# Performance work log

Measured on AMD Instinct MI355X. Metric: run time of the kernel, lower is better.

The kernel has to match this reference:

```python
import jax, jax.numpy as jnp
import numpy as np
from jax import lax
from jax.scipy.linalg import solve_triangular

SR = 16000
FRAME_PERIOD = 80
FFT_LENGTH = 1024
WIN_MS = 30
EPS = 1e-05
DEFAULT_F0 = 150.0
B, T, N = 8, 320000, 4000

N_BAND = int(np.log2(SR / 600))  # 4
CUTOFF = [SR / 2 ** i for i in range(2, N_BAND + 1)]
CUTOFF.append(CUTOFF[-1])  # [4000, 2000, 1000, 1000]
SEG = [int(c * WIN_MS / 500 + 1.5) for c in CUTOFF]  # [241, 121, 61, 61]

_HHP_VALS = [0.00041447996898231424, 0.0007812505141729248, -0.0010917236836275842,
             -0.001986792567596759, 0.0020903896961562292, 0.004094057027284935,
             -0.0034025808529816698, -0.007496154127205602, 0.004972263339933064,
             0.012738791249119802, -0.006696032689574911, -0.020694051570247052,
             0.008432436565041345, 0.03307438375870053, -0.010018936738799522,
             -0.05423136140580825, 0.011293988915051487, 0.10020081367388213,
             -0.012120546202484579, -0.316300210390957, 0.5124068258062764]
_HLP_VALS = [-0.0006548817007748305, 7.561994958159384e-05, 0.0020408456937895227,
             -0.0007468053532203044, -0.004350223568826493, 0.0025966428382642732,
             0.007639602282756696, -0.006490411890149785, -0.011765804538954506,
             0.013649908479276255, 0.01636866479016021, -0.026075976030529347,
             -0.020910294856659444, 0.04826072503231665, 0.02476784661104811,
             -0.09617846758336064, -0.027359756709866623, 0.3148805216163004,
             0.5282734359405503]

def _qmf_high():
    h = np.zeros(41)
    h[:21] = _HHP_VALS
    h[21:] = h[19::-1]
    return h.astype(np.float32)

def _qmf_low():
    h = np.zeros(37)
    h[:19] = _HLP_VALS
    h[19:] = h[17::-1]
    return h.astype(np.float32)

def _make_window():
    w = np.zeros((N_BAND, SEG[0]), np.float32)
    for i, s in enumerate(SEG):
        w[i, :s] = np.hanning(s + 2)[1:-1]
    return w

def _interp_tables():
    coarse = np.concatenate([[0.0], [SR / 2 ** i for i in range(N_BAND, 0, -1)]])
    freq = np.arange(FFT_LENGTH // 2 + 1) * (SR / FFT_LENGTH)
    idx = np.clip(np.searchsorted(coarse, freq) - 1, 0, len(coarse) - 2)
    x0 = coarse[:-1]
    dx = coarse[1:] - x0
    wts = ((freq - x0[idx]) / dx[idx]).astype(np.float32)
    return idx.astype(np.int32), wts

_HHP = _qmf_high()
_HLP = _qmf_low()
_WIN = _make_window()
_IDX, _WTS = _interp_tables()


def _qmf_conv(x, h):
    # x: (B, T), h: (k,). Reflection pad k//2, cross-correlation, stride 2.
    p = h.shape[0] // 2
    xp = jnp.pad(x, ((0, 0), (p, p)), mode='reflect')
    out = lax.conv_general_dilated(xp[:, None, :], h[None, None, :], (2,), 'VALID',
                                   dimension_numbers=('NCH', 'OIH', 'NCH'))
    return out[:, 0, :]


def setup_inputs() -> dict:
    key = jax.random.key(0)
    k1, k2 = jax.random.split(key)
    x = jax.random.normal(k1, (B, T), jnp.float32)
    f0 = 100.0 + 200.0 * jax.random.uniform(k2, (B, N), jnp.float32)  # 100-300 Hz
    return {"x": x, "f0": f0}


def reference(x, f0):
    hHP = jnp.asarray(_HHP)
    hLP = jnp.asarray(_HLP)
    f0 = lax.stop_gradient(jnp.where(f0 <= 32, DEFAULT_F0, f0))
    Bn, Nf = f0.shape
    time_axis = jnp.arange(Nf, dtype=f0.dtype) * (FRAME_PERIOD / SR)
    bidx = jnp.arange(Bn)[:, None, None]
    eye6 = EPS * jnp.eye(6, dtype=x.dtype)
    lx = x
    bap = []
    for i in range(N_BAND):
        if i < N_BAND - 1:
            hx = _qmf_conv(lx, hHP)
            lx = _qmf_conv(lx, hLP)
            xb = hx
        else:
            xb = lx
        seg = SEG[i]
        tmp_fs = 2.0 * CUTOFF[i]
        pitch = tmp_fs / f0
        t0 = (pitch + 0.5).astype(jnp.int32)
        index_bias = (pitch * 0.5 + 0.5).astype(jnp.int32)
        curr_pos = (time_axis * tmp_fs + 1.5).astype(jnp.int32)[None, :]
        origin = curr_pos - index_bias  # (B, N)
        j = jnp.arange(-1, seg + 1)  # (seg+2,)
        T1 = xb.shape[-1] - 1
        ia = jnp.clip((origin - t0)[..., None] + j, 0, T1)
        ib = jnp.clip((origin + t0)[..., None] + j, 0, T1)
        Ha = xb[bidx, ia]  # (B, N, seg+2)
        Hb = xb[bidx, ib]

        def unfold3(a):  # size-3 sliding windows -> (B, N, seg, 3)
            return jnp.stack([a[..., 0:seg], a[..., 1:seg + 1], a[..., 2:seg + 2]], axis=-1)

        H = jnp.concatenate([unfold3(Ha), unfold3(Hb)], axis=-1)  # (B, N, seg, 6)
        w = jnp.asarray(_WIN[i, :seg])
        Hw = jnp.swapaxes(H, -2, -1) * w  # (B, N, 6, seg)
        R = Hw @ H  # (B, N, 6, 6)
        ig = jnp.clip(origin[..., None] + j[1:-1], 0, T1)
        X = xb[bidx, ig][..., None]  # (B, N, seg, 1)
        L = jnp.linalg.cholesky(R + eye6)
        b = Hw @ X  # (B, N, 6, 1)
        y1 = solve_triangular(L, b, lower=True)
        a = solve_triangular(jnp.swapaxes(L, -2, -1), y1, lower=False)
        HaX = H @ a  # (B, N, seg, 1)
        wsqrt = jnp.sqrt(w)
        wx = wsqrt * X[..., 0]
        wxHa = wsqrt * (X - HaX)[..., 0]
        A = jnp.std(wxHa, axis=-1, ddof=1) / (jnp.std(wx, axis=-1, ddof=1) + 1e-16)
        bap.append(A)
    bap.append(bap[-1])
    ap = jnp.stack(bap[::-1], axis=-1)  # (B, N, n_band+1), low->high freq
    # piecewise-linear interpolation in log domain onto fft bins
    y = jnp.log(ap)
    y0 = y[..., :-1]
    dy = y[..., 1:] - y0
    yi = jnp.take(dy, jnp.asarray(_IDX), axis=-1) * jnp.asarray(_WTS) \
         + jnp.take(y0, jnp.asarray(_IDX), axis=-1)
    return jnp.exp(yi)  # (B, N, fft//2+1)
```

## Files before the change

kernel.cpp:

```cpp
#include <hip/hip_runtime.h>
#include <math.h>

#define NB 8
#define NF 4000
#define NFRAMES (NB * NF)

__constant__ float c_hhp[21] = {
    0.00041447996898231424, 0.0007812505141729248, -0.0010917236836275842,
    -0.001986792567596759,  0.0020903896961562292, 0.004094057027284935,
    -0.0034025808529816698, -0.007496154127205602, 0.004972263339933064,
    0.012738791249119802,   -0.006696032689574911, -0.020694051570247052,
    0.008432436565041345,   0.03307438375870053,   -0.010018936738799522,
    -0.05423136140580825,   0.011293988915051487,  0.10020081367388213,
    -0.012120546202484579,  -0.316300210390957,    0.5124068258062764};
__constant__ float c_hlp[19] = {
    -0.0006548817007748305, 7.561994958159384e-05, 0.0020408456937895227,
    -0.0007468053532203044, -0.004350223568826493, 0.0025966428382642732,
    0.007639602282756696,   -0.006490411890149785, -0.011765804538954506,
    0.013649908479276255,   0.01636866479016021,   -0.026075976030529347,
    -0.020910294856659444,  0.04826072503231665,   0.02476784661104811,
    -0.09617846758336064,   -0.027359756709866623, 0.3148805216163004,
    0.5282734359405503};

__device__ __forceinline__ int reflidx(int i, int len) {
  if (i < 0) i = -i;
  if (i >= len) i = 2 * len - 2 - i;
  return i;
}
__device__ __forceinline__ int clampi(int i, int hi) {
  return min(max(i, 0), hi);
}

__global__ __launch_bounds__(256) void qmf_kernel(
    const float* __restrict__ in, int len, float* __restrict__ outH,
    float* __restrict__ outL, float2* __restrict__ wtab) {
  int half = len >> 1;
  int gid = blockIdx.x * 256 + threadIdx.x;
  if (gid >= NB * half) {
    if (wtab) {
      const int segs[4] = {241, 121, 61, 61};
      int k = threadIdx.x;
      for (int i = 0; i < 4; ++i) {
        float v = 0.f;
        if (k < segs[i]) {
          double ang = 2.0 * 3.14159265358979323846 * (double)(k + 1) /
                       (double)(segs[i] + 1);
          v = (float)(0.5 - 0.5 * cos(ang));
        }
        wtab[i * 256 + k] = make_float2(v, sqrtf(v));
      }
    }
    return;
  }
  int b = gid / half;
  int nn = gid - b * half;
  const float* row = in + (size_t)b * len;
  int c = 2 * nn;
  float sh = 0.f, sl = 0.f;
  if (c >= 20 && c <= len - 22) {
    const float2* p2 = reinterpret_cast<const float2*>(row + (c - 20));
    float v[42];
#pragma unroll
    for (int j = 0; j < 21; ++j) {
      float2 t = p2[j];
      v[2 * j] = t.x;
      v[2 * j + 1] = t.y;
    }
#pragma unroll
    for (int t = 0; t < 41; ++t) sh += v[t] * c_hhp[t <= 20 ? t : 40 - t];
#pragma unroll
    for (int t = 0; t < 37; ++t) sl += v[t + 2] * c_hlp[t <= 18 ? t : 36 - t];
  } else {
#pragma unroll
    for (int t = 0; t < 41; ++t)
      sh += row[reflidx(c + t - 20, len)] * c_hhp[t <= 20 ? t : 40 - t];
#pragma unroll
    for (int t = 0; t < 37; ++t)
      sl += row[reflidx(c + t - 18, len)] * c_hlp[t <= 18 ? t : 36 - t];
  }
  outH[(size_t)b * half + nn] = sh;
  outL[(size_t)b * half + nn] = sl;
}

#define ACCUM_SAMPLE()                         \
  do {                                         \
    sxx += wk * x * x;                         \
    s1x += wsk * x;                            \
    float wh0 = wk * h0, wh1 = wk * h1, wh2 = wk * h2, wh3 = wk * h3, \
          wh4 = wk * h4, wh5 = wk * h5;        \
    gv[0] += wsk * h0; gv[1] += wsk * h1; gv[2] += wsk * h2;          \
    gv[3] += wsk * h3; gv[4] += wsk * h4; gv[5] += wsk * h5;          \
    bv[0] += wh0 * x;  bv[1] += wh1 * x;  bv[2] += wh2 * x;           \
    bv[3] += wh3 * x;  bv[4] += wh4 * x;  bv[5] += wh5 * x;           \
    rr[0] += wh0 * h0;  rr[1] += wh0 * h1;  rr[2] += wh0 * h2;        \
    rr[3] += wh0 * h3;  rr[4] += wh0 * h4;  rr[5] += wh0 * h5;        \
    rr[6] += wh1 * h1;  rr[7] += wh1 * h2;  rr[8] += wh1 * h3;        \
    rr[9] += wh1 * h4;  rr[10] += wh1 * h5; rr[11] += wh2 * h2;       \
    rr[12] += wh2 * h3; rr[13] += wh2 * h4; rr[14] += wh2 * h5;       \
    rr[15] += wh3 * h3; rr[16] += wh3 * h4; rr[17] += wh3 * h5;       \
    rr[18] += wh4 * h4; rr[19] += wh4 * h5; rr[20] += wh5 * h5;       \
  } while (0)

template <int GS, int NITER, bool CLAMP>
__device__ __forceinline__ void acc_loop(
    const float* __restrict__ row, int T1, int base_a, int base_b, int origin,
    int sub, const float2* __restrict__ wtab, float rr[21], float bv[6],
    float gv[6], float& sxx, float& s1x) {
  if (!CLAMP) {
    const float* pa = row + base_a + sub;
    const float* pb = row + base_b + sub;
    const float* pg = row + origin + sub;
    const float2* pw = wtab + sub;
#pragma unroll 4
    for (int j = 0; j < NITER; ++j) {
      float2 wp = pw[j * GS];
      float wk = wp.x, wsk = wp.y;
      float h0 = pa[j * GS], h1 = pa[j * GS + 1], h2 = pa[j * GS + 2];
      float h3 = pb[j * GS], h4 = pb[j * GS + 1], h5 = pb[j * GS + 2];
      float x = pg[j * GS];
      ACCUM_SAMPLE();
    }
  } else {
#pragma unroll 4
    for (int j = 0; j < NITER; ++j) {
      int k = sub + j * GS;
      float2 wp = wtab[k];
      float wk = wp.x, wsk = wp.y;
      int ia = base_a + k, ib = base_b + k;
      float h0 = row[clampi(ia, T1)];
      float h1 = row[clampi(ia + 1, T1)];
      float h2 = row[clampi(ia + 2, T1)];
      float h3 = row[clampi(ib, T1)];
      float h4 = row[clampi(ib + 1, T1)];
      float h5 = row[clampi(ib + 2, T1)];
      float x = row[clampi(origin + k, T1)];
      ACCUM_SAMPLE();
    }
  }
}

template <int SEG, int LGS, int NITER>
__device__ __forceinline__ void band_body(
    const float* __restrict__ xb, int bandLen, const float* __restrict__ f0,
    float tmp_fs, const float2* __restrict__ wtab, float* __restrict__ Aout,
    int blk) {
  constexpr int GS = 1 << LGS;
  constexpr int FPB = 256 / GS;
  constexpr int KMAX = NITER * GS;
  const int sub = threadIdx.x & (GS - 1);
  const int frame = blk * FPB + (threadIdx.x >> LGS);
  const int b = frame / NF;
  const int n = frame - b * NF;

  float f0v = f0[frame];
  if (f0v <= 32.0f) f0v = 150.0f;
  float pitch = tmp_fs / f0v;
  int t0 = (int)(__fadd_rn(pitch, 0.5f));
  int ibias = (int)(__fadd_rn(__fmul_rn(pitch, 0.5f), 0.5f));
  float tt = __fmul_rn((float)n, 0.005f);
  int curr = (int)(__fadd_rn(__fmul_rn(tt, tmp_fs), 1.5f));
  int origin = curr - ibias;
  const int T1 = bandLen - 1;
  const float* row = xb + (size_t)b * bandLen;
  const int base_a = origin - t0 - 1;
  const int base_b = origin + t0 - 1;

  float rr[21], bv[6], gv[6], sxx = 0.f, s1x = 0.f;
#pragma unroll
  for (int i = 0; i < 21; ++i) rr[i] = 0.f;
#pragma unroll
  for (int i = 0; i < 6; ++i) bv[i] = 0.f;
#pragma unroll
  for (int i = 0; i < 6; ++i) gv[i] = 0.f;

  const bool fast = (base_a >= 0) && (base_b + KMAX + 1 <= T1);
  if (fast)
    acc_loop<GS, NITER, false>(row, T1, base_a, base_b, origin, sub, wtab, rr,
                               bv, gv, sxx, s1x);
  else
    acc_loop<GS, NITER, true>(row, T1, base_a, base_b, origin, sub, wtab, rr,
                              bv, gv, sxx, s1x);

#pragma unroll
  for (int off = GS / 2; off >= 1; off >>= 1) {
#pragma unroll
    for (int i = 0; i < 21; ++i) rr[i] += __shfl_xor(rr[i], off, 64);
#pragma unroll
    for (int i = 0; i < 6; ++i) bv[i] += __shfl_xor(bv[i], off, 64);
    sxx += __shfl_xor(sxx, off, 64);
    s1x += __shfl_xor(s1x, off, 64);
  }

  float M[6][6], invd[6];
  {
    int c = 0;
#pragma unroll
    for (int p = 0; p < 6; ++p)
#pragma unroll
      for (int q = p; q < 6; ++q) {
        M[p][q] = rr[c];
        M[q][p] = rr[c];
        ++c;
      }
#pragma unroll
    for (int p = 0; p < 6; ++p) M[p][p] += 1e-5f;
  }
#pragma unroll
  for (int p = 0; p < 6; ++p) {
    float d = M[p][p];
#pragma unroll
    for (int j = 0; j < 6; ++j)
      if (j < p) d -= M[p][j] * M[p][j];
    d = sqrtf(d);
    M[p][p] = d;
    float inv = 1.0f / d;
    invd[p] = inv;
#pragma unroll
    for (int q = 0; q < 6; ++q)
      if (q > p) {
        float s = M[q][p];
#pragma unroll
        for (int j = 0; j < 6; ++j)
          if (j < p) s -= M[q][j] * M[p][j];
        M[q][p] = s * inv;
      }
  }
  float yv[6], av[6];
#pragma unroll
  for (int p = 0; p < 6; ++p) {
    float s = bv[p];
#pragma unroll
    for (int j = 0; j < 6; ++j)
      if (j < p) s -= M[p][j] * yv[j];
    yv[p] = s * invd[p];
  }
#pragma unroll
  for (int p = 5; p >= 0; --p) {
    float s = yv[p];
#pragma unroll
    for (int j = 0; j < 6; ++j)
      if (j > p) s -= M[j][p] * av[j];
    av[p] = s * invd[p];
  }

  float adotg = av[0] * gv[0] + av[1] * gv[1] + av[2] * gv[2] +
                av[3] * gv[3] + av[4] * gv[4] + av[5] * gv[5];
#pragma unroll
  for (int off = GS / 2; off >= 1; off >>= 1)
    adotg += __shfl_xor(adotg, off, 64);

  float adotb = 0.f, quad = 0.f;
  {
    int c = 0;
#pragma unroll
    for (int p = 0; p < 6; ++p) {
      adotb += av[p] * bv[p];
#pragma unroll
      for (int q = p; q < 6; ++q) {
        float t = av[p] * av[q] * rr[c++];
        quad += (q == p) ? t : 2.f * t;
      }
    }
  }
  if (sub == 0) {
    float s2r = sxx - 2.f * adotb + quad;
    float s1r = s1x - adotg;
    const float nf = (float)SEG;
    float vx = (sxx - s1x * s1x / nf) / (nf - 1.0f);
    float vr = (s2r - s1r * s1r / nf) / (nf - 1.0f);
    float sx = sqrtf(fmaxf(vx, 0.f));
    float sr = sqrtf(fmaxf(vr, 0.f));
    Aout[frame] = sr / (sx + 1e-16f);
  }
}

__global__ __launch_bounds__(256) void bands_kernel(
    const float* __restrict__ hx0, const float* __restrict__ hx1,
    const float* __restrict__ hx2, const float* __restrict__ lx2,
    const float* __restrict__ f0, const float2* __restrict__ wtab,
    float* __restrict__ Aarr) {
  int blk = blockIdx.x;
  if (blk < 1000) {
    band_body<241, 3, 32>(hx0, 160000, f0, 8000.0f, wtab + 0 * 256,
                          Aarr + 0 * NFRAMES, blk);
  } else if (blk < 2000) {
    band_body<121, 3, 16>(hx1, 80000, f0, 4000.0f, wtab + 1 * 256,
                          Aarr + 1 * NFRAMES, blk - 1000);
  } else if (blk < 2500) {
    band_body<61, 2, 16>(hx2, 40000, f0, 2000.0f, wtab + 2 * 256,
                         Aarr + 2 * NFRAMES, blk - 2000);
  } else {
    band_body<61, 2, 16>(lx2, 40000, f0, 2000.0f, wtab + 3 * 256,
                         Aarr + 3 * NFRAMES, blk - 2500);
  }
}

__global__ __launch_bounds__(256) void interp_kernel(
    const float* __restrict__ A, float* __restrict__ out) {
  const int wave = threadIdx.x >> 6;
  const int lane = threadIdx.x & 63;
  const int f = blockIdx.x * 4 + wave;
  float l0 = __logf(A[0 * NFRAMES + f]);
  float l1 = __logf(A[1 * NFRAMES + f]);
  float l2 = __logf(A[2 * NFRAMES + f]);
  float l3 = __logf(A[3 * NFRAMES + f]);
  float d1 = l2 - l3, d2 = l1 - l2, d3 = l0 - l1;
  float* orow = out + (size_t)f * 513;
  for (int k = lane; k < 513; k += 64) {
    float y0, dy, c;
    int k0;
    if (k <= 64) {
      y0 = l3; dy = 0.f; k0 = 0; c = 0.015625f;
    } else if (k <= 128) {
      y0 = l3; dy = d1; k0 = 64; c = 0.015625f;
    } else if (k <= 256) {
      y0 = l2; dy = d2; k0 = 128; c = 0.0078125f;
    } else {
      y0 = l1; dy = d3; k0 = 256; c = 0.00390625f;
    }
    float w = (float)(k - k0) * c;
    orow[k] = __expf(y0 + w * dy);
  }
}

extern "C" void kernel_launch(void* const* d_in, const int* in_sizes, int n_in,
                              void* d_out, int out_size, void* d_ws,
                              size_t ws_size, hipStream_t stream) {
  const float* x = (const float*)d_in[0];
  const float* f0 = (const float*)d_in[1];
  float* out = (float*)d_out;
  float* ws = (float*)d_ws;

  float* hx0 = ws + 0;
  float* lx0 = hx0 + 1280000;
  float* hx1 = lx0 + 1280000;
  float* lx1 = hx1 + 640000;
  float* hx2 = lx1 + 640000;
  float* lx2 = hx2 + 320000;
  float* Aarr = lx2 + 320000;
  float2* wtab = (float2*)(Aarr + 4 * NFRAMES);
  (void)ws_size;

  hipLaunchKernelGGL(qmf_kernel, dim3(5000), dim3(256), 0, stream, x, 320000,
                     hx0, lx0, (float2*)nullptr);
  hipLaunchKernelGGL(qmf_kernel, dim3(2500), dim3(256), 0, stream, lx0,
                     160000, hx1, lx1, (float2*)nullptr);
  hipLaunchKernelGGL(qmf_kernel, dim3(1251), dim3(256), 0, stream, lx1, 80000,
                     hx2, lx2, wtab);

  hipLaunchKernelGGL(bands_kernel, dim3(3000), dim3(256), 0, stream, hx0, hx1,
                     hx2, lx2, f0, wtab, Aarr);

  hipLaunchKernelGGL(interp_kernel, dim3(NFRAMES / 4), dim3(256), 0, stream,
                     Aarr, out);
}
```

Before: 81.87 us.

## Stage per-block signal window and window table in LDS for band accumulation

```diff
diff --git a/kernel.cpp b/kernel.cpp
--- a/kernel.cpp
+++ b/kernel.cpp
@@ -101,56 +101,24 @@
     rr[18] += wh4 * h4; rr[19] += wh4 * h5; rr[20] += wh5 * h5;       \
   } while (0)
 
-template <int GS, int NITER, bool CLAMP>
-__device__ __forceinline__ void acc_loop(
-    const float* __restrict__ row, int T1, int base_a, int base_b, int origin,
-    int sub, const float2* __restrict__ wtab, float rr[21], float bv[6],
-    float gv[6], float& sxx, float& s1x) {
-  if (!CLAMP) {
-    const float* pa = row + base_a + sub;
-    const float* pb = row + base_b + sub;
-    const float* pg = row + origin + sub;
-    const float2* pw = wtab + sub;
-#pragma unroll 4
-    for (int j = 0; j < NITER; ++j) {
-      float2 wp = pw[j * GS];
-      float wk = wp.x, wsk = wp.y;
-      float h0 = pa[j * GS], h1 = pa[j * GS + 1], h2 = pa[j * GS + 2];
-      float h3 = pb[j * GS], h4 = pb[j * GS + 1], h5 = pb[j * GS + 2];
-      float x = pg[j * GS];
-      ACCUM_SAMPLE();
-    }
-  } else {
-#pragma unroll 4
-    for (int j = 0; j < NITER; ++j) {
-      int k = sub + j * GS;
-      float2 wp = wtab[k];
-      float wk = wp.x, wsk = wp.y;
-      int ia = base_a + k, ib = base_b + k;
-      float h0 = row[clampi(ia, T1)];
-      float h1 = row[clampi(ia + 1, T1)];
-      float h2 = row[clampi(ia + 2, T1)];
-      float h3 = row[clampi(ib, T1)];
-      float h4 = row[clampi(ib + 1, T1)];
-      float h5 = row[clampi(ib + 2, T1)];
-      float x = row[clampi(origin + k, T1)];
-      ACCUM_SAMPLE();
-    }
-  }
-}
+#define LDS_SIG_CAP 1792
 
 template <int SEG, int LGS, int NITER>
 __device__ __forceinline__ void band_body(
     const float* __restrict__ xb, int bandLen, const float* __restrict__ f0,
-    float tmp_fs, const float2* __restrict__ wtab, float* __restrict__ Aout,
-    int blk) {
+    float tmp_fs, const float2* __restrict__ wtab_g, float* __restrict__ Aout,
+    int blk, float* __restrict__ lds_sig, float2* __restrict__ lds_w,
+    int* __restrict__ sred) {
   constexpr int GS = 1 << LGS;
   constexpr int FPB = 256 / GS;
   constexpr int KMAX = NITER * GS;
-  const int sub = threadIdx.x & (GS - 1);
-  const int frame = blk * FPB + (threadIdx.x >> LGS);
+  const int tid = threadIdx.x;
+  const int sub = tid & (GS - 1);
+  const int frame = blk * FPB + (tid >> LGS);
   const int b = frame / NF;
   const int n = frame - b * NF;
+
+  lds_w[tid] = wtab_g[tid];
 
   float f0v = f0[frame];
   if (f0v <= 32.0f) f0v = 150.0f;
@@ -165,6 +133,27 @@
   const int base_a = origin - t0 - 1;
   const int base_b = origin + t0 - 1;
 
+  int lo = base_a;
+  int hi = origin + t0 + KMAX + 2;
+#pragma unroll
+  for (int off = 32; off >= 1; off >>= 1) {
+    lo = min(lo, __shfl_xor(lo, off, 64));
+    hi = max(hi, __shfl_xor(hi, off, 64));
+  }
+  if ((tid & 63) == 0) {
+    sred[tid >> 6] = lo;
+    sred[4 + (tid >> 6)] = hi;
+  }
+  __syncthreads();
+  int blo = min(min(sred[0], sred[1]), min(sred[2], sred[3]));
+  int bhi = max(max(sred[4], sred[5]), max(sred[6], sred[7]));
+  const bool ldsok =
+      (blo >= 0) && (bhi <= bandLen) && (bhi - blo <= LDS_SIG_CAP);
+  if (ldsok) {
+    for (int i = tid; i < bhi - blo; i += 256) lds_sig[i] = row[blo + i];
+  }
+  __syncthreads();
+
   float rr[21], bv[6], gv[6], sxx = 0.f, s1x = 0.f;
 #pragma unroll
   for (int i = 0; i < 21; ++i) rr[i] = 0.f;
@@ -173,13 +162,37 @@
 #pragma unroll
   for (int i = 0; i < 6; ++i) gv[i] = 0.f;
 
-  const bool fast = (base_a >= 0) && (base_b + KMAX + 1 <= T1);
-  if (fast)
-    acc_loop<GS, NITER, false>(row, T1, base_a, base_b, origin, sub, wtab, rr,
-                               bv, gv, sxx, s1x);
-  else
-    acc_loop<GS, NITER, true>(row, T1, base_a, base_b, origin, sub, wtab, rr,
-                              bv, gv, sxx, s1x);
+  if (ldsok) {
+    const float* pa = lds_sig + (base_a - blo) + sub;
+    const float* pb = lds_sig + (base_b - blo) + sub;
+    const float* pg = lds_sig + (origin - blo) + sub;
+    const float2* pw = lds_w + sub;
+#pragma unroll 4
+    for (int j = 0; j < NITER; ++j) {
+      float2 wp = pw[j * GS];
+      float wk = wp.x, wsk = wp.y;
+      float h0 = pa[j * GS], h1 = pa[j * GS + 1], h2 = pa[j * GS + 2];
+      float h3 = pb[j * GS], h4 = pb[j * GS + 1], h5 = pb[j * GS + 2];
+      float x = pg[j * GS];
+      ACCUM_SAMPLE();
+    }
+  } else {
+#pragma unroll 4
+    for (int j = 0; j < NITER; ++j) {
+      int k = sub + j * GS;
+      float2 wp = lds_w[k];
+      float wk = wp.x, wsk = wp.y;
+      int ia = base_a + k, ib = base_b + k;
+      float h0 = row[clampi(ia, T1)];
+      float h1 = row[clampi(ia + 1, T1)];
+      float h2 = row[clampi(ia + 2, T1)];
+      float h3 = row[clampi(ib, T1)];
+      float h4 = row[clampi(ib + 1, T1)];
+      float h5 = row[clampi(ib + 2, T1)];
+      float x = row[clampi(origin + k, T1)];
+      ACCUM_SAMPLE();
+    }
+  }
 
 #pragma unroll
   for (int off = GS / 2; off >= 1; off >>= 1) {
@@ -279,19 +292,23 @@
     const float* __restrict__ hx2, const float* __restrict__ lx2,
     const float* __restrict__ f0, const float2* __restrict__ wtab,
     float* __restrict__ Aarr) {
+  __shared__ float lds_sig[LDS_SIG_CAP];
+  __shared__ float2 lds_w[256];
+  __shared__ int sred[8];
   int blk = blockIdx.x;
   if (blk < 1000) {
     band_body<241, 3, 32>(hx0, 160000, f0, 8000.0f, wtab + 0 * 256,
-                          Aarr + 0 * NFRAMES, blk);
+                          Aarr + 0 * NFRAMES, blk, lds_sig, lds_w, sred);
   } else if (blk < 2000) {
     band_body<121, 3, 16>(hx1, 80000, f0, 4000.0f, wtab + 1 * 256,
-                          Aarr + 1 * NFRAMES, blk - 1000);
-  } else if (blk < 2500) {
-    band_body<61, 2, 16>(hx2, 40000, f0, 2000.0f, wtab + 2 * 256,
-                         Aarr + 2 * NFRAMES, blk - 2000);
+                          Aarr + 1 * NFRAMES, blk - 1000, lds_sig, lds_w,
+                          sred);
+  } else if (blk < 3000) {
+    band_body<61, 3, 8>(hx2, 40000, f0, 2000.0f, wtab + 2 * 256,
+                        Aarr + 2 * NFRAMES, blk - 2000, lds_sig, lds_w, sred);
   } else {
-    band_body<61, 2, 16>(lx2, 40000, f0, 2000.0f, wtab + 3 * 256,
-                         Aarr + 3 * NFRAMES, blk - 2500);
+    band_body<61, 3, 8>(lx2, 40000, f0, 2000.0f, wtab + 3 * 256,
+                        Aarr + 3 * NFRAMES, blk - 3000, lds_sig, lds_w, sred);
   }
 }
 
@@ -348,7 +365,7 @@
   hipLaunchKernelGGL(qmf_kernel, dim3(1251), dim3(256), 0, stream, lx1, 80000,
                      hx2, lx2, wtab);
 
-  hipLaunchKernelGGL(bands_kernel, dim3(3000), dim3(256), 0, stream, hx0, hx1,
+  hipLaunchKernelGGL(bands_kernel, dim3(4000), dim3(256), 0, stream, hx0, hx1,
                      hx2, lx2, f0, wtab, Aarr);
 
   hipLaunchKernelGGL(interp_kernel, dim3(NFRAMES / 4), dim3(256), 0, stream,
```

Measured after the change: 88.62 us. 1.08x slower.

## Split per-frame Cholesky solve into separate kernel using staged sufficient statistics

Applied to the files above, without the earlier changes.

```diff
diff --git a/kernel.cpp b/kernel.cpp
--- a/kernel.cpp
+++ b/kernel.cpp
@@ -4,6 +4,7 @@
 #define NB 8
 #define NF 4000
 #define NFRAMES (NB * NF)
+#define TOTF (4 * NFRAMES)
 
 __constant__ float c_hhp[21] = {
     0.00041447996898231424, 0.0007812505141729248, -0.0010917236836275842,
@@ -142,7 +143,7 @@
 template <int SEG, int LGS, int NITER>
 __device__ __forceinline__ void band_body(
     const float* __restrict__ xb, int bandLen, const float* __restrict__ f0,
-    float tmp_fs, const float2* __restrict__ wtab, float* __restrict__ Aout,
+    float tmp_fs, const float2* __restrict__ wtab, float* __restrict__ sums_col,
     int blk) {
   constexpr int GS = 1 << LGS;
   constexpr int FPB = 256 / GS;
@@ -187,9 +188,56 @@
     for (int i = 0; i < 21; ++i) rr[i] += __shfl_xor(rr[i], off, 64);
 #pragma unroll
     for (int i = 0; i < 6; ++i) bv[i] += __shfl_xor(bv[i], off, 64);
+#pragma unroll
+    for (int i = 0; i < 6; ++i) gv[i] += __shfl_xor(gv[i], off, 64);
     sxx += __shfl_xor(sxx, off, 64);
     s1x += __shfl_xor(s1x, off, 64);
   }
+
+  if (sub == 0) {
+    float* sp = sums_col + frame;
+#pragma unroll
+    for (int i = 0; i < 21; ++i) sp[(size_t)i * TOTF] = rr[i];
+#pragma unroll
+    for (int i = 0; i < 6; ++i) sp[(size_t)(21 + i) * TOTF] = bv[i];
+#pragma unroll
+    for (int i = 0; i < 6; ++i) sp[(size_t)(27 + i) * TOTF] = gv[i];
+    sp[(size_t)33 * TOTF] = sxx;
+    sp[(size_t)34 * TOTF] = s1x;
+  }
+}
+
+__global__ __launch_bounds__(256) void bands_kernel(
+    const float* __restrict__ hx0, const float* __restrict__ hx1,
+    const float* __restrict__ hx2, const float* __restrict__ lx2,
+    const float* __restrict__ f0, const float2* __restrict__ wtab,
+    float* __restrict__ sums) {
+  int blk = blockIdx.x;
+  if (blk < 1000) {
+    band_body<241, 3, 32>(hx0, 160000, f0, 8000.0f, wtab + 0 * 256,
+                          sums + 0 * NFRAMES, blk);
+  } else if (blk < 2000) {
+    band_body<121, 3, 16>(hx1, 80000, f0, 4000.0f, wtab + 1 * 256,
+                          sums + 1 * NFRAMES, blk - 1000);
+  } else if (blk < 2500) {
+    band_body<61, 2, 16>(hx2, 40000, f0, 2000.0f, wtab + 2 * 256,
+                         sums + 2 * NFRAMES, blk - 2000);
+  } else {
+    band_body<61, 2, 16>(lx2, 40000, f0, 2000.0f, wtab + 3 * 256,
+                         sums + 3 * NFRAMES, blk - 2500);
+  }
+}
+
+__global__ __launch_bounds__(256) void solve_kernel(
+    const float* __restrict__ sums, float* __restrict__ Aarr) {
+  const int t = blockIdx.x * 256 + threadIdx.x;
+  float v[35];
+#pragma unroll
+  for (int i = 0; i < 35; ++i) v[i] = sums[(size_t)i * TOTF + t];
+  const float nf = (t >= 2 * NFRAMES) ? 61.0f
+                   : (t >= NFRAMES)   ? 121.0f
+                                      : 241.0f;
+  float sxx = v[33], s1x = v[34];
 
   float M[6][6], invd[6];
   {
@@ -198,8 +246,8 @@
     for (int p = 0; p < 6; ++p)
 #pragma unroll
       for (int q = p; q < 6; ++q) {
-        M[p][q] = rr[c];
-        M[q][p] = rr[c];
+        M[p][q] = v[c];
+        M[q][p] = v[c];
         ++c;
       }
 #pragma unroll
@@ -228,7 +276,7 @@
   float yv[6], av[6];
 #pragma unroll
   for (int p = 0; p < 6; ++p) {
-    float s = bv[p];
+    float s = v[21 + p];
 #pragma unroll
     for (int j = 0; j < 6; ++j)
       if (j < p) s -= M[p][j] * yv[j];
@@ -243,56 +291,27 @@
     av[p] = s * invd[p];
   }
 
-  float adotg = av[0] * gv[0] + av[1] * gv[1] + av[2] * gv[2] +
-                av[3] * gv[3] + av[4] * gv[4] + av[5] * gv[5];
-#pragma unroll
-  for (int off = GS / 2; off >= 1; off >>= 1)
-    adotg += __shfl_xor(adotg, off, 64);
-
-  float adotb = 0.f, quad = 0.f;
+  float adotb = 0.f, adotg = 0.f, quad = 0.f;
   {
     int c = 0;
 #pragma unroll
     for (int p = 0; p < 6; ++p) {
-      adotb += av[p] * bv[p];
+      adotb += av[p] * v[21 + p];
+      adotg += av[p] * v[27 + p];
 #pragma unroll
       for (int q = p; q < 6; ++q) {
-        float t = av[p] * av[q] * rr[c++];
-        quad += (q == p) ? t : 2.f * t;
+        float tt = av[p] * av[q] * v[c++];
+        quad += (q == p) ? tt : 2.f * tt;
       }
     }
   }
-  if (sub == 0) {
-    float s2r = sxx - 2.f * adotb + quad;
-    float s1r = s1x - adotg;
-    const float nf = (float)SEG;
-    float vx = (sxx - s1x * s1x / nf) / (nf - 1.0f);
-    float vr = (s2r - s1r * s1r / nf) / (nf - 1.0f);
-    float sx = sqrtf(fmaxf(vx, 0.f));
-    float sr = sqrtf(fmaxf(vr, 0.f));
-    Aout[frame] = sr / (sx + 1e-16f);
-  }
-}
-
-__global__ __launch_bounds__(256) void bands_kernel(
-    const float* __restrict__ hx0, const float* __restrict__ hx1,
-    const float* __restrict__ hx2, const float* __restrict__ lx2,
-    const float* __restrict__ f0, const float2* __restrict__ wtab,
-    float* __restrict__ Aarr) {
-  int blk = blockIdx.x;
-  if (blk < 1000) {
-    band_body<241, 3, 32>(hx0, 160000, f0, 8000.0f, wtab + 0 * 256,
-                          Aarr + 0 * NFRAMES, blk);
-  } else if (blk < 2000) {
-    band_body<121, 3, 16>(hx1, 80000, f0, 4000.0f, wtab + 1 * 256,
-                          Aarr + 1 * NFRAMES, blk - 1000);
-  } else if (blk < 2500) {
-    band_body<61, 2, 16>(hx2, 40000, f0, 2000.0f, wtab + 2 * 256,
-                         Aarr + 2 * NFRAMES, blk - 2000);
-  } else {
-    band_body<61, 2, 16>(lx2, 40000, f0, 2000.0f, wtab + 3 * 256,
-                         Aarr + 3 * NFRAMES, blk - 2500);
-  }
+  float s2r = sxx - 2.f * adotb + quad;
+  float s1r = s1x - adotg;
+  float vx = (sxx - s1x * s1x / nf) / (nf - 1.0f);
+  float vr = (s2r - s1r * s1r / nf) / (nf - 1.0f);
+  float sx = sqrtf(fmaxf(vx, 0.f));
+  float sr = sqrtf(fmaxf(vr, 0.f));
+  Aarr[t] = sr / (sx + 1e-16f);
 }
 
 __global__ __launch_bounds__(256) void interp_kernel(
@@ -339,6 +358,7 @@
   float* lx2 = hx2 + 320000;
   float* Aarr = lx2 + 320000;
   float2* wtab = (float2*)(Aarr + 4 * NFRAMES);
+  float* sums = (float*)(wtab + 4 * 256);
   (void)ws_size;
 
   hipLaunchKernelGGL(qmf_kernel, dim3(5000), dim3(256), 0, stream, x, 320000,
@@ -349,7 +369,10 @@
                      hx2, lx2, wtab);
 
   hipLaunchKernelGGL(bands_kernel, dim3(3000), dim3(256), 0, stream, hx0, hx1,
-                     hx2, lx2, f0, wtab, Aarr);
+                     hx2, lx2, f0, wtab, sums);
+
+  hipLaunchKernelGGL(solve_kernel, dim3(TOTF / 256), dim3(256), 0, stream,
+                     sums, Aarr);
 
   hipLaunchKernelGGL(interp_kernel, dim3(NFRAMES / 4), dim3(256), 0, stream,
                      Aarr, out);
```

Result: slower. 85.02 us (+3.8%).
